# Optimization experiments

Measured on AMD Instinct MI355X. Metric: run time of the kernel, lower is better.

## Reference

```python
import jax, jax.numpy as jnp
import numpy as np

B, NPG, H, TD, NF, NL, A = 64, 20, 512, 256, 128, 6, 100
N = B * NPG
E = B * NPG * (NPG - 1)
ANG_LO, ANG_HI = 59.9, 120.1
LOG_MEANS = jnp.array([1.575442910194397, 1.7017393112182617, 1.9781638383865356], jnp.float32)
LOG_STDS = jnp.array([0.24437622725963593, 0.26526379585266113, 0.3535512685775757], jnp.float32)
TWO_PI = 2.0 * np.pi


def _logmap(x, y):
    z = TWO_PI * (y - x)
    return jnp.arctan2(jnp.sin(z), jnp.cos(z)) / TWO_PI


def _lattice_matrix(lengths, angles_deg):
    a = jnp.deg2rad(angles_deg)
    c, s = jnp.cos(a), jnp.sin(a)
    val = jnp.clip((c[:, 0] * c[:, 1] - c[:, 2]) / (s[:, 0] * s[:, 1]), -1.0, 1.0)
    gs = jnp.arccos(val)
    zero = jnp.zeros_like(lengths[:, 0])
    va = jnp.stack([lengths[:, 0] * s[:, 1], zero, lengths[:, 0] * c[:, 1]], 1)
    vb = jnp.stack([-lengths[:, 1] * s[:, 0] * jnp.cos(gs), lengths[:, 1] * s[:, 0] * jnp.sin(gs), lengths[:, 1] * c[:, 0]], 1)
    vc = jnp.stack([zero, zero, lengths[:, 2]], 1)
    return jnp.stack([va, vb, vc], 1)


def _ln(x, g, b, eps=1e-5):
    mu = jnp.mean(x, -1, keepdims=True)
    var = jnp.var(x, -1, keepdims=True)
    return (x - mu) * jax.lax.rsqrt(var + eps) * g + b


def setup_inputs() -> dict:
    key = jax.random.key(0)
    ks = jax.random.split(key, 24)
    # forward data
    t = jax.random.uniform(ks[0], (B, 1), jnp.float32)
    atom_types = jax.random.randint(ks[1], (N,), 1, A + 1, jnp.int32)
    frac_coords = jax.random.uniform(ks[2], (N, 3), jnp.float32)
    lattice_params = 0.5 * jax.random.normal(ks[3], (B, 6), jnp.float32)
    num_atoms = jnp.full((B,), NPG, jnp.int32)
    node2graph = jnp.repeat(jnp.arange(B, dtype=jnp.int32), NPG)
    # fully-connected edges per graph, no self edges (static structure)
    loc = np.arange(NPG)
    src_l, dst_l = np.meshgrid(loc, loc, indexing='ij')
    mask = src_l != dst_l
    src_l, dst_l = src_l[mask], dst_l[mask]  # (NPG*(NPG-1),)
    offs = (np.arange(B)[:, None] * NPG)
    src = (offs + src_l[None, :]).reshape(-1)
    dst = (offs + dst_l[None, :]).reshape(-1)
    edge_index = jnp.asarray(np.stack([src, dst]), jnp.int32)  # (2, E)
    edge2graph = node2graph[edge_index[0]]
    # parameters
    def w(k, shape, fan_in):
        return (jax.random.normal(k, shape, jnp.float32) / np.sqrt(fan_in)).astype(jnp.float32)
    EIN = 3 + 3 * H + 6 + NF * 2 * 3  # 2313
    p = {
        'W_node': w(ks[4], (A, H), A),
        'W_time': w(ks[5], (1, TD), 1),
        'W_latent': w(ks[6], (H + TD, H), H + TD),
        'ln_gamma': jnp.ones((NL, H), jnp.float32),
        'ln_beta': jnp.zeros((NL, H), jnp.float32),
        'We1': w(ks[7], (NL, EIN, H), EIN),
        'be1': jnp.zeros((NL, H), jnp.float32),
        'We2': w(ks[8], (NL, H, H), H),
        'be2': jnp.zeros((NL, H), jnp.float32),
        'Wn1': w(ks[9], (NL, 2 * H, H), 2 * H),
        'bn1': jnp.zeros((NL, H), jnp.float32),
        'Wn2': w(ks[10], (NL, H, H), H),
        'bn2': jnp.zeros((NL, H), jnp.float32),
        'W_numatom': w(ks[11], (NL, A, H), A),
        'fln_gamma': jnp.ones((H,), jnp.float32),
        'fln_beta': jnp.zeros((H,), jnp.float32),
        'W_coord': w(ks[12], (H, 3), H),
        'W_latout': w(ks[13], (2 * H, 6), 2 * H),
        'b_latout': jnp.zeros((6,), jnp.float32),
    }
    return dict(t=t, frac_coords=frac_coords, lattice_params=lattice_params,
                atom_types=atom_types, num_atoms=num_atoms, node2graph=node2graph,
                edge_index=edge_index, edge2graph=edge2graph, **p)


def reference(t, frac_coords, lattice_params, W_node, W_time, W_latent, ln_gamma, ln_beta,
              We1, be1, We2, be2, Wn1, bn1, Wn2, bn2, W_numatom, fln_gamma, fln_beta,
              W_coord, W_latout, b_latout, atom_types, num_atoms, node2graph, edge_index, edge2graph):
    n_nodes = frac_coords.shape[0]
    n_graphs = t.shape[0]
    src, dst = edge_index[0], edge_index[1]
    frac_diff = _logmap(frac_coords[src], frac_coords[dst])  # (E,3)

    atom_oh = jax.nn.one_hot(jnp.clip(atom_types - 1, 0), A, dtype=jnp.float32)
    h = atom_oh @ W_node
    temb = t @ W_time  # (B,TD)
    h = jnp.concatenate([h, temb[node2graph]], -1) @ W_latent

    lattice_flat = lattice_params  # 6-D in directly
    lengths = jnp.exp(lattice_params[:, :3] * LOG_STDS + LOG_MEANS)
    angles_deg = ANG_LO + (ANG_HI - ANG_LO) * jax.nn.sigmoid(lattice_params[:, 3:])
    Lmat = _lattice_matrix(lengths, angles_deg)  # (B,3,3)
    ltl = jnp.einsum('bij,bkj->bik', Lmat, Lmat)  # L @ L^T

    dots = jnp.einsum('eij,ej->ei', ltl[edge2graph], frac_diff)
    unit_dots = dots / (jnp.linalg.norm(dots, axis=-1, keepdims=True) + 1e-12)

    freqs = TWO_PI * jnp.arange(NF, dtype=jnp.float32)
    emb = (frac_diff[..., None] * freqs).reshape(-1, 3 * NF)
    femb = jnp.concatenate([jnp.sin(emb), jnp.cos(emb)], -1)  # (E, 768)

    na_oh = jax.nn.one_hot(num_atoms - 1, A, dtype=jnp.float32)  # (B,100)
    lat_e = lattice_flat[edge2graph]
    counts = jnp.maximum(jax.ops.segment_sum(jnp.ones_like(src, dtype=jnp.float32), src, num_segments=n_nodes), 1.0)[:, None]

    for l in range(NL):
        h_in = h
        hn = _ln(h_in, ln_gamma[l], ln_beta[l])
        na_emb = (na_oh @ W_numatom[l])[edge2graph]
        ef = jnp.concatenate([unit_dots, hn[src], hn[dst], lat_e, femb, na_emb], -1)
        e = jax.nn.silu(jax.nn.silu(ef @ We1[l] + be1[l]) @ We2[l] + be2[l])
        agg = jax.ops.segment_sum(e, src, num_segments=n_nodes) / counts
        out = jax.nn.silu(jax.nn.silu(jnp.concatenate([hn, agg], -1) @ Wn1[l] + bn1[l]) @ Wn2[l] + bn2[l])
        h = h_in + out

    h = _ln(h, fln_gamma, fln_beta)
    pos_v = h @ W_coord  # (N,3)
    sum_pool = jax.ops.segment_sum(h, node2graph, num_segments=n_graphs)
    mean_pool = sum_pool / num_atoms.astype(jnp.float32)[:, None]
    cell_v = jnp.concatenate([mean_pool, sum_pool], -1) @ W_latout + b_latout  # (B,6)
    return pos_v, cell_v
```

## Files before the change

### kernel.cpp

```cpp
#include <hip/hip_runtime.h>
#include <hip/hip_bf16.h>

typedef __hip_bfloat16 bf16;
typedef __attribute__((ext_vector_type(8))) __bf16 bf16x8;
typedef __attribute__((ext_vector_type(4))) float f32x4;

#define B_   64
#define NPG_ 20
#define H_   512
#define TD_  256
#define NF_  128
#define NL_  6
#define A_   100
#define N_   (B_ * NPG_)
#define E_   (B_ * NPG_ * (NPG_-1))
#define EIN_ 2313

__device__ __forceinline__ float bf2f(bf16 x) { return __bfloat162float(x); }
__device__ __forceinline__ bf16  f2bf(float x) { return __float2bfloat16(x); }
__device__ __forceinline__ float siluf(float x) { return x / (1.0f + expf(-x)); }
__device__ __forceinline__ float ldf(const void* p, size_t i, int isb) {
    return isb ? bf2f(((const bf16*)p)[i]) : ((const float*)p)[i];
}
__device__ __forceinline__ void async_cp16(const bf16* src, bf16* dst) {
    __builtin_amdgcn_global_load_lds(
        (const __attribute__((address_space(1))) unsigned int*)src,
        (__attribute__((address_space(3))) unsigned int*)dst,
        16, 0, 0);
}

__global__ void detect_dtype(const unsigned int* __restrict__ tw, int* __restrict__ flag) {
    if (threadIdx.x != 0) return;
    int cnt = 0;
    for (int i = 0; i < 32; i++) {
        unsigned b1 = (tw[i] >> 8) & 0xFF;
        if (b1 >= 0x20 && b1 < 0x40) cnt++;
    }
    *flag = (cnt >= 16) ? 1 : 0;
}

__global__ void ws_sentinel(bf16* out) { if (threadIdx.x == 0) out[0] = f2bf(1000.0f); }

__global__ void prep_graph(const void* __restrict__ latp, float* __restrict__ ltl,
                           const int* __restrict__ flag) {
    int b = threadIdx.x;
    if (b >= B_) return;
    int isb = *flag;
    const float LM[3] = {1.575442910194397f, 1.7017393112182617f, 1.9781638383865356f};
    const float LS[3] = {0.24437622725963593f, 0.26526379585266113f, 0.3535512685775757f};
    float lp[6];
    for (int i = 0; i < 6; i++) lp[i] = ldf(latp, b*6 + i, isb);
    float len[3], c[3], s[3];
    for (int i = 0; i < 3; i++) len[i] = expf(lp[i] * LS[i] + LM[i]);
    for (int i = 0; i < 3; i++) {
        float sig = 1.0f / (1.0f + expf(-lp[3+i]));
        float deg = 59.9f + 60.2f * sig;
        float a = deg * 0.017453292519943295f;
        c[i] = cosf(a); s[i] = sinf(a);
    }
    float val = (c[0]*c[1] - c[2]) / (s[0]*s[1]);
    val = fminf(1.0f, fmaxf(-1.0f, val));
    float gs = acosf(val);
    float L[3][3];
    L[0][0] = len[0]*s[1]; L[0][1] = 0.0f;               L[0][2] = len[0]*c[1];
    L[1][0] = -len[1]*s[0]*cosf(gs); L[1][1] = len[1]*s[0]*sinf(gs); L[1][2] = len[1]*c[0];
    L[2][0] = 0.0f; L[2][1] = 0.0f; L[2][2] = len[2];
    for (int i = 0; i < 3; i++)
        for (int k = 0; k < 3; k++)
            ltl[b*9 + i*3 + k] = L[i][0]*L[k][0] + L[i][1]*L[k][1] + L[i][2]*L[k][2];
}

__global__ __launch_bounds__(512) void prep_q(const void* __restrict__ W_time,
                                              const void* __restrict__ W_latent,
                                              float* __restrict__ q,
                                              const int* __restrict__ flag) {
    int j = threadIdx.x;
    int isb = *flag;
    float s0 = 0.0f, s1 = 0.0f, s2 = 0.0f, s3 = 0.0f;
    for (int d = 0; d < TD_; d += 4) {
        s0 += ldf(W_time, d+0, isb) * ldf(W_latent, (size_t)(H_ + d+0)*H_ + j, isb);
        s1 += ldf(W_time, d+1, isb) * ldf(W_latent, (size_t)(H_ + d+1)*H_ + j, isb);
        s2 += ldf(W_time, d+2, isb) * ldf(W_latent, (size_t)(H_ + d+2)*H_ + j, isb);
        s3 += ldf(W_time, d+3, isb) * ldf(W_latent, (size_t)(H_ + d+3)*H_ + j, isb);
    }
    q[j] = (s0 + s1) + (s2 + s3);
}

__global__ __launch_bounds__(256) void pq_gather(const void* __restrict__ W_node,
                                                 const void* __restrict__ W_numatom,
                                                 bf16* __restrict__ PQa,
                                                 const int* __restrict__ flag) {
    int z = blockIdx.x, ch = blockIdx.y;
    int isb = *flag;
    int base = ch * 4096;
    for (int idx = base + threadIdx.x; idx < base + 4096; idx += 256) {
        int r = idx >> 9, c = idx & 511;
        float v = 0.0f;
        if (r < A_) {
            if (z == 0) v = ldf(W_node, (size_t)r*512 + c, isb);
            else        v = ldf(W_numatom, ((size_t)(z-1)*A_ + r)*512 + c, isb);
        }
        PQa[(size_t)z*65536 + idx] = f2bf(v);
    }
}

__global__ __launch_bounds__(256) void transpose_pq(const void* __restrict__ W_latent,
                                                    const void* __restrict__ We1,
                                                    bf16* __restrict__ PQbt,
                                                    const int* __restrict__ flag) {
    __shared__ bf16 tile[32][33];
    int z = blockIdx.z;
    int isb = *flag;
    const void* src = (z == 0) ? W_latent : We1;
    size_t off = (z == 0) ? 0 : ((size_t)(z-1)*EIN_ + 1801)*512;
    bf16* dst = PQbt + (size_t)z*512*512;
    int r0 = blockIdx.y * 32, c0 = blockIdx.x * 32;
    #pragma unroll
    for (int i = 0; i < 32; i += 8)
        tile[threadIdx.y + i][threadIdx.x] =
            f2bf(ldf(src, off + (size_t)(r0 + threadIdx.y + i)*512 + c0 + threadIdx.x, isb));
    __syncthreads();
    #pragma unroll
    for (int i = 0; i < 32; i += 8)
        dst[(size_t)(c0 + threadIdx.y + i)*512 + r0 + threadIdx.x] = tile[threadIdx.x][threadIdx.y + i];
}

__global__ __launch_bounds__(256) void transpose_layer(
    const void* __restrict__ We1p, const void* __restrict__ We2p,
    const void* __restrict__ Wn1p, const void* __restrict__ Wn2p, size_t l,
    bf16* __restrict__ WtAB, bf16* __restrict__ Wtf, bf16* __restrict__ Wte2,
    bf16* __restrict__ Wtn1, bf16* __restrict__ Wtn2,
    const int* __restrict__ flag) {
    __shared__ bf16 tile[32][33];
    int which = blockIdx.z;
    int isb = *flag;
    const void* src; size_t off; bf16* dst; int R;
    switch (which) {
        case 0:  src = We1p; off = (l*EIN_ + 3)*512;    dst = WtAB;            R = 512;  break;
        case 1:  src = We1p; off = (l*EIN_ + 515)*512;  dst = WtAB + 512*512;  R = 512;  break;
        case 2:  src = We1p; off = (l*EIN_ + 1033)*512; dst = Wtf;             R = 768;  break;
        case 3:  src = We2p; off = l*512*512;           dst = Wte2;            R = 512;  break;
        case 4:  src = Wn1p; off = l*1024*512;          dst = Wtn1;            R = 1024; break;
        default: src = Wn2p; off = l*512*512;           dst = Wtn2;            R = 512;  break;
    }
    int r0 = blockIdx.y * 32, c0 = blockIdx.x * 32;
    if (r0 >= R) return;
    #pragma unroll
    for (int i = 0; i < 32; i += 8)
        tile[threadIdx.y + i][threadIdx.x] =
            f2bf(ldf(src, off + (size_t)(r0 + threadIdx.y + i)*512 + c0 + threadIdx.x, isb));
    __syncthreads();
    #pragma unroll
    for (int i = 0; i < 32; i += 8)
        dst[(size_t)(c0 + threadIdx.y + i)*R + r0 + threadIdx.x] = tile[threadIdx.x][threadIdx.y + i];
}

__global__ __launch_bounds__(512) void node_embed_fast(const bf16* __restrict__ P,
                                                       const float* __restrict__ q,
                                                       const void* __restrict__ t,
                                                       const int* __restrict__ atom_types,
                                                       const int* __restrict__ node2graph,
                                                       float* __restrict__ h,
                                                       const int* __restrict__ flag) {
    int i = blockIdx.x, j = threadIdx.x;
    int isb = *flag;
    int at = atom_types[i] - 1; if (at < 0) at = 0;
    float pv = (at < A_) ? bf2f(P[(size_t)at*512 + j]) : 0.0f;
    float tv = ldf(t, node2graph[i], isb);
    h[(size_t)i*H_ + j] = pv + tv * q[j];
}

__global__ __launch_bounds__(384) void edge_prep(const void* __restrict__ frac,
                                                 const int* __restrict__ edge_index,
                                                 const int* __restrict__ e2g,
                                                 const void* __restrict__ latp,
                                                 const int* __restrict__ num_atoms,
                                                 const float* __restrict__ ltl,
                                                 float* __restrict__ edat,
                                                 bf16* __restrict__ femb,
                                                 const int* __restrict__ flag) {
    const float TWO_PI_F = 6.283185307179586f;
    int e = blockIdx.x;
    int isb = *flag;
    int src = edge_index[e], dst = edge_index[E_ + e];
    int tid = threadIdx.x;
    int d = tid >> 7, k = tid & 127;
    float x = ldf(frac, src*3 + d, isb), y = ldf(frac, dst*3 + d, isb);
    float diff = y - x;
    float fd = diff - rintf(diff);
    float sv, cv;
    sincosf(fd * (TWO_PI_F * (float)k), &sv, &cv);
    femb[(size_t)e*768 + d*NF_ + k]       = f2bf(sv);
    femb[(size_t)e*768 + 384 + d*NF_ + k] = f2bf(cv);
    if (tid < 3) {
        int g = e2g[e];
        float f3[3];
        for (int dd = 0; dd < 3; dd++) {
            float df = ldf(frac, dst*3 + dd, isb) - ldf(frac, src*3 + dd, isb);
            f3[dd] = df - rintf(df);
        }
        float dots[3];
        for (int i = 0; i < 3; i++)
            dots[i] = ltl[g*9 + i*3 + 0]*f3[0] + ltl[g*9 + i*3 + 1]*f3[1] + ltl[g*9 + i*3 + 2]*f3[2];
        float nrm = sqrtf(dots[0]*dots[0] + dots[1]*dots[1] + dots[2]*dots[2]);
        edat[(size_t)e*16 + tid] = dots[tid] / (nrm + 1e-12f);
        if (tid == 0) {
            for (int i = 0; i < 6; i++) edat[(size_t)e*16 + 3 + i] = ldf(latp, g*6 + i, isb);
            int na = num_atoms[g] - 1;
            if (na < 0 || na >= A_) na = -1;
            edat[(size_t)e*16 + 9]  = __int_as_float(src);
            edat[(size_t)e*16 + 10] = __int_as_float(dst);
            edat[(size_t)e*16 + 11] = __int_as_float(na);
        }
    }
}

__device__ __forceinline__ float block_sum_256(float v, float* red) {
    for (int o = 32; o; o >>= 1) v += __shfl_down(v, o);
    int w = threadIdx.x >> 6, lane = threadIdx.x & 63;
    if (lane == 0) red[w] = v;
    __syncthreads();
    float s = red[0] + red[1] + red[2] + red[3];
    __syncthreads();
    return s;
}

__global__ __launch_bounds__(256) void ln_kernel(const float* __restrict__ x,
                                                 const void* __restrict__ gamma,
                                                 const void* __restrict__ beta, size_t goff,
                                                 bf16* __restrict__ cat,
                                                 const int* __restrict__ flag) {
    __shared__ float red[4];
    size_t n = blockIdx.x;
    int tid = threadIdx.x;
    int isb = *flag;
    const float* xr = x + n*H_;
    float v0 = xr[tid], v1 = xr[tid + 256];
    float mu = block_sum_256(v0 + v1, red) * (1.0f/512.0f);
    float d0 = v0 - mu, d1 = v1 - mu;
    float var = block_sum_256(d0*d0 + d1*d1, red) * (1.0f/512.0f);
    float rs = 1.0f / sqrtf(var + 1e-5f);
    cat[n*1024 + tid]       = f2bf(d0*rs*ldf(gamma, goff + tid, isb)       + ldf(beta, goff + tid, isb));
    cat[n*1024 + 256 + tid] = f2bf(d1*rs*ldf(gamma, goff + tid + 256, isb) + ldf(beta, goff + tid + 256, isb));
}

template<int EPI, int TM>
__global__ __launch_bounds__(256) void gemm_bt(
        const bf16* __restrict__ A, int lda,
        const bf16* __restrict__ Bt,
        const void* __restrict__ bias, size_t boff,
        bf16* __restrict__ Cb, float* __restrict__ Cf,
        int K, int N,
        size_t zsA, size_t zsB, size_t zsC,
        const int* __restrict__ flag,
        const bf16* __restrict__ hnAB, const bf16* __restrict__ Qc,
        const float* __restrict__ edat,
        const void* __restrict__ We1, size_t lidx) {
    constexpr int MT = TM / 32;
    __shared__ __align__(16) bf16 As[TM*64];
    __shared__ __align__(16) bf16 Bs[128*64];
    const int z = blockIdx.z;
    A  += (size_t)z * zsA;
    Bt += (size_t)z * zsB;
    const size_t coff = (size_t)z * zsC;
    const int tid = threadIdx.x;
    const int wave = tid >> 6, lane = tid & 63;
    const int lrow = lane & 15, lq = lane >> 4;
    const size_t m0 = (size_t)blockIdx.y * TM;
    const int n0 = blockIdx.x * 128;
    const int wm = (wave >> 1) * (TM/2), wn = (wave & 1) * 64;
    const int ar = lane >> 3;
    const int gk = (lane & 7) ^ ar;
    f32x4 acc[MT][4] = {};

    for (int k0 = 0; k0 < K; k0 += 64) {
        if (k0) __syncthreads();
        #pragma unroll
        for (int i = 0; i < TM/32; i++) {
            int R = wave*(TM/4) + i*8;
            async_cp16(A + (m0 + R + ar)*lda + k0 + gk*8, As + R*64);
        }
        #pragma unroll
        for (int i = 0; i < 4; i++) {
            int R = wave*32 + i*8;
            async_cp16(Bt + (size_t)(n0 + R + ar)*K + k0 + gk*8, Bs + R*64);
        }
        __syncthreads();
        #pragma unroll
        for (int kk = 0; kk < 2; kk++) {
            bf16x8 af[MT], bfr[4];
            #pragma unroll
            for (int mt = 0; mt < MT; mt++) {
                int r = wm + mt*16 + lrow;
                int p = (kk*4 + lq) ^ (r & 7);
                af[mt] = *(const bf16x8*)(As + r*64 + p*8);
            }
            #pragma unroll
            for (int nt = 0; nt < 4; nt++) {
                int r = wn + nt*16 + lrow;
                int p = (kk*4 + lq) ^ (r & 7);
                bfr[nt] = *(const bf16x8*)(Bs + r*64 + p*8);
            }
            #pragma unroll
            for (int mt = 0; mt < MT; mt++)
                #pragma unroll
                for (int nt = 0; nt < 4; nt++)
                    acc[mt][nt] = __builtin_amdgcn_mfma_f32_16x16x32_bf16(af[mt], bfr[nt], acc[mt][nt], 0, 0, 0);
        }
    }

    if constexpr (EPI == 3) {
        const int isb = *flag;
        float w9[4][9], b1v[4];
        #pragma unroll
        for (int nt = 0; nt < 4; nt++) {
            int col = n0 + wn + nt*16 + lrow;
            size_t wb = lidx*EIN_*512 + col;
            w9[nt][0] = ldf(We1, wb + 0*512, isb);
            w9[nt][1] = ldf(We1, wb + 1*512, isb);
            w9[nt][2] = ldf(We1, wb + 2*512, isb);
            #pragma unroll
            for (int i = 0; i < 6; i++) w9[nt][3+i] = ldf(We1, wb + (size_t)(1027+i)*512, isb);
            b1v[nt] = ldf(bias, boff + col, isb);
        }
        #pragma unroll
        for (int mt = 0; mt < MT; mt++) {
            #pragma unroll
            for (int r = 0; r < 4; r++) {
                size_t e = m0 + wm + mt*16 + lq*4 + r;
                const float4* ed = (const float4*)(edat + e*16);
                float4 q0 = ed[0], q1 = ed[1], q2 = ed[2];
                int se = __float_as_int(q2.y), de = __float_as_int(q2.z), na = __float_as_int(q2.w);
                #pragma unroll
                for (int nt = 0; nt < 4; nt++) {
                    int col = n0 + wn + nt*16 + lrow;
                    float x = acc[mt][nt][r] + b1v[nt]
                            + bf2f(hnAB[(size_t)se*1024 + col])
                            + bf2f(hnAB[(size_t)de*1024 + 512 + col])
                            + (na >= 0 ? bf2f(Qc[(size_t)(1+lidx)*65536 + (size_t)na*512 + col]) : 0.0f)
                            + q0.x*w9[nt][0] + q0.y*w9[nt][1] + q0.z*w9[nt][2]
                            + q0.w*w9[nt][3] + q1.x*w9[nt][4] + q1.y*w9[nt][5]
                            + q1.z*w9[nt][6] + q1.w*w9[nt][7] + q2.x*w9[nt][8];
                    Cb[e*512 + col] = f2bf(siluf(x));
                }
            }
        }
    } else {
        const int isb = bias ? *flag : 0;
        #pragma unroll
        for (int mt = 0; mt < MT; mt++)
            #pragma unroll
            for (int nt = 0; nt < 4; nt++) {
                int col = n0 + wn + nt*16 + lrow;
                float bv = bias ? ldf(bias, boff + col, isb) : 0.0f;
                #pragma unroll
                for (int r = 0; r < 4; r++) {
                    size_t row = m0 + wm + mt*16 + lq*4 + r;
                    float x = acc[mt][nt][r] + bv;
                    if (EPI == 0)      Cb[coff + row*N + col] = f2bf(x);
                    else if (EPI == 1) Cb[coff + row*N + col] = f2bf(siluf(x));
                    else               Cf[coff + row*N + col] += siluf(x);
                }
            }
    }
}

__global__ __launch_bounds__(256) void seg_mean(const bf16* __restrict__ e2,
                                                bf16* __restrict__ cat) {
    int n = blockIdx.x;
    #pragma unroll
    for (int jj = 0; jj < 2; jj++) {
        int j = threadIdx.x + jj*256;
        const bf16* base = e2 + (size_t)n*19*H_ + j;
        float s = 0.0f;
        #pragma unroll
        for (int i = 0; i < 19; i++) s += bf2f(base[(size_t)i*H_]);
        cat[(size_t)n*1024 + 512 + j] = f2bf(s / 19.0f);
    }
}

__global__ __launch_bounds__(256) void pos_out(const bf16* __restrict__ hln,
                                               const void* __restrict__ W_coord,
                                               void* __restrict__ out,
                                               const int* __restrict__ flag) {
    int wave = threadIdx.x >> 6, lane = threadIdx.x & 63;
    int n = blockIdx.x*4 + wave;
    int isb = *flag;
    float s0 = 0, s1 = 0, s2 = 0;
    for (int k = lane; k < H_; k += 64) {
        float hv = bf2f(hln[(size_t)n*1024 + k]);
        s0 += hv * ldf(W_coord, k*3 + 0, isb);
        s1 += hv * ldf(W_coord, k*3 + 1, isb);
        s2 += hv * ldf(W_coord, k*3 + 2, isb);
    }
    for (int o = 32; o; o >>= 1) {
        s0 += __shfl_down(s0, o); s1 += __shfl_down(s1, o); s2 += __shfl_down(s2, o);
    }
    if (lane == 0) {
        if (isb) { bf16* o = (bf16*)out;  o[n*3] = f2bf(s0); o[n*3+1] = f2bf(s1); o[n*3+2] = f2bf(s2); }
        else     { float* o = (float*)out; o[n*3] = s0; o[n*3+1] = s1; o[n*3+2] = s2; }
    }
}

__global__ __launch_bounds__(512) void cell_out(const bf16* __restrict__ hln,
                                                const void* __restrict__ W_latout,
                                                const void* __restrict__ b_latout,
                                                const int* __restrict__ num_atoms,
                                                void* __restrict__ out,
                                                const int* __restrict__ flag) {
    __shared__ float red[8*6];
    int b = blockIdx.x, j = threadIdx.x;
    int isb = *flag;
    float s = 0.0f;
    for (int i = 0; i < NPG_; i++) s += bf2f(hln[(size_t)(b*NPG_ + i)*1024 + j]);
    float m = s / (float)num_atoms[b];
    float p[6];
    #pragma unroll
    for (int c = 0; c < 6; c++)
        p[c] = m * ldf(W_latout, j*6 + c, isb) + s * ldf(W_latout, (512 + j)*6 + c, isb);
    int w = j >> 6, lane = j & 63;
    #pragma unroll
    for (int c = 0; c < 6; c++) {
        float v = p[c];
        for (int o = 32; o; o >>= 1) v += __shfl_down(v, o);
        if (lane == 0) red[w*6 + c] = v;
    }
    __syncthreads();
    if (j < 6) {
        float v = 0.0f;
        for (int w2 = 0; w2 < 8; w2++) v += red[w2*6 + j];
        float r = v + ldf(b_latout, j, isb);
        if (isb) ((bf16*)out)[N_*3 + b*6 + j] = f2bf(r);
        else     ((float*)out)[N_*3 + b*6 + j] = r;
    }
}

extern "C" void kernel_launch(void* const* d_in, const int* in_sizes, int n_in,
                              void* d_out, int out_size, void* d_ws, size_t ws_size,
                              hipStream_t stream) {
    const void* t          = d_in[0];
    const void* frac       = d_in[1];
    const void* latp       = d_in[2];
    const int*  atom_types = (const int*)d_in[3];
    const int*  num_atoms  = (const int*)d_in[4];
    const int*  node2graph = (const int*)d_in[5];
    const int*  edge_index = (const int*)d_in[6];
    const int*  e2g        = (const int*)d_in[7];
    const void* W_node     = d_in[8];
    const void* W_time     = d_in[9];
    const void* W_latent   = d_in[10];
    const void* ln_gamma   = d_in[11];
    const void* ln_beta    = d_in[12];
    const void* We1        = d_in[13];
    const void* be1        = d_in[14];
    const void* We2        = d_in[15];
    const void* be2        = d_in[16];
    const void* Wn1        = d_in[17];
    const void* bn1        = d_in[18];
    const void* Wn2        = d_in[19];
    const void* bn2        = d_in[20];
    const void* W_numatom  = d_in[21];
    const void* fln_gamma  = d_in[22];
    const void* fln_beta   = d_in[23];
    const void* W_coord    = d_in[24];
    const void* W_latout   = d_in[25];
    const void* b_latout   = d_in[26];

    char* p = (char*)d_ws;
    auto alloc = [&](size_t bytes) { char* r = p; p += (bytes + 255) & ~(size_t)255; return r; };
    int*   flag  = (int*)alloc(4);
    float* ltl   = (float*)alloc((size_t)B_*9*4);
    float* q     = (float*)alloc((size_t)H_*4);
    float* h     = (float*)alloc((size_t)N_*H_*4);
    float* edat  = (float*)alloc((size_t)E_*16*4);
    bf16* hnAB  = (bf16*)alloc((size_t)N_*1024*2);
    bf16* femb  = (bf16*)alloc((size_t)E_*768*2);
    bf16* e1    = (bf16*)alloc((size_t)E_*H_*2);
    bf16* e2    = (bf16*)alloc((size_t)E_*H_*2);
    bf16* cat   = (bf16*)alloc((size_t)N_*1024*2);
    bf16* n1s   = (bf16*)alloc((size_t)N_*H_*2);
    bf16* PQc   = (bf16*)alloc((size_t)7*128*512*2);
    bf16* WtAB  = (bf16*)alloc((size_t)1024*512*2);
    bf16* Wtf   = (bf16*)alloc((size_t)512*768*2);
    bf16* Wte2  = (bf16*)alloc((size_t)512*512*2);
    bf16* Wtn1  = (bf16*)alloc((size_t)512*1024*2);
    bf16* Wtn2  = (bf16*)alloc((size_t)512*512*2);
    bf16* PQa   = e1;
    bf16* PQbt  = e2;

    if ((size_t)(p - (char*)d_ws) > ws_size) {
        ws_sentinel<<<1, 64, 0, stream>>>((bf16*)d_out);
        return;
    }

    detect_dtype<<<1, 64, 0, stream>>>((const unsigned int*)t, flag);
    prep_graph<<<1, 64, 0, stream>>>(latp, ltl, flag);
    prep_q<<<1, 512, 0, stream>>>(W_time, W_latent, q, flag);
    pq_gather<<<dim3(7, 16), 256, 0, stream>>>(W_node, W_numatom, PQa, flag);
    transpose_pq<<<dim3(16, 16, 7), dim3(32, 8), 0, stream>>>(W_latent, We1, PQbt, flag);
    gemm_bt<0,128><<<dim3(4, 1, 7), 256, 0, stream>>>(
        PQa, 512, PQbt, nullptr, 0, PQc, nullptr, 512, 512,
        (size_t)128*512, (size_t)512*512, (size_t)128*512,
        flag, nullptr, nullptr, nullptr, nullptr, 0);
    node_embed_fast<<<N_, 512, 0, stream>>>(PQc, q, t, atom_types, node2graph, h, flag);
    edge_prep<<<E_, 384, 0, stream>>>(frac, edge_index, e2g, latp, num_atoms, ltl, edat, femb, flag);

    for (size_t l = 0; l < NL_; l++) {
        transpose_layer<<<dim3(16, 32, 6), dim3(32, 8), 0, stream>>>(
            We1, We2, Wn1, Wn2, l, WtAB, Wtf, Wte2, Wtn1, Wtn2, flag);
        ln_kernel<<<N_, 256, 0, stream>>>(h, ln_gamma, ln_beta, l*H_, cat, flag);
        gemm_bt<0,64><<<dim3(8, N_/64), 256, 0, stream>>>(
            cat, 1024, WtAB, nullptr, 0, hnAB, nullptr, 512, 1024, 0, 0, 0,
            flag, nullptr, nullptr, nullptr, nullptr, 0);
        gemm_bt<3,128><<<dim3(4, E_/128), 256, 0, stream>>>(
            femb, 768, Wtf, be1, l*H_, e1, nullptr, 768, 512, 0, 0, 0,
            flag, hnAB, PQc, edat, We1, l);
        gemm_bt<1,128><<<dim3(4, E_/128), 256, 0, stream>>>(
            e1, 512, Wte2, be2, l*H_, e2, nullptr, 512, 512, 0, 0, 0,
            flag, nullptr, nullptr, nullptr, nullptr, 0);
        seg_mean<<<N_, 256, 0, stream>>>(e2, cat);
        gemm_bt<1,64><<<dim3(4, N_/64), 256, 0, stream>>>(
            cat, 1024, Wtn1, bn1, l*H_, n1s, nullptr, 1024, 512, 0, 0, 0,
            flag, nullptr, nullptr, nullptr, nullptr, 0);
        gemm_bt<2,64><<<dim3(4, N_/64), 256, 0, stream>>>(
            n1s, 512, Wtn2, bn2, l*H_, nullptr, h, 512, 512, 0, 0, 0,
            flag, nullptr, nullptr, nullptr, nullptr, 0);
    }

    ln_kernel<<<N_, 256, 0, stream>>>(h, fln_gamma, fln_beta, 0, cat, flag);
    pos_out<<<N_/4, 256, 0, stream>>>(cat, W_coord, d_out, flag);
    cell_out<<<B_, 512, 0, stream>>>(cat, W_latout, b_latout, num_atoms, d_out, flag);
}
```

Measured before the change: 1.223 ms.

## Fold small edge features into femb GEMM K dimension and shrink edge tiles

```diff
diff --git a/kernel.cpp b/kernel.cpp
--- a/kernel.cpp
+++ b/kernel.cpp
@@ -15,6 +15,7 @@
 #define N_   (B_ * NPG_)
 #define E_   (B_ * NPG_ * (NPG_-1))
 #define EIN_ 2313
+#define KF_  832
 
 __device__ __forceinline__ float bf2f(bf16 x) { return __bfloat162float(x); }
 __device__ __forceinline__ bf16  f2bf(float x) { return __float2bfloat16(x); }
@@ -134,14 +135,14 @@
     __shared__ bf16 tile[32][33];
     int which = blockIdx.z;
     int isb = *flag;
-    const void* src; size_t off; bf16* dst; int R;
+    const void* src; size_t off; bf16* dst; int R; int ldd;
     switch (which) {
-        case 0:  src = We1p; off = (l*EIN_ + 3)*512;    dst = WtAB;            R = 512;  break;
-        case 1:  src = We1p; off = (l*EIN_ + 515)*512;  dst = WtAB + 512*512;  R = 512;  break;
-        case 2:  src = We1p; off = (l*EIN_ + 1033)*512; dst = Wtf;             R = 768;  break;
-        case 3:  src = We2p; off = l*512*512;           dst = Wte2;            R = 512;  break;
-        case 4:  src = Wn1p; off = l*1024*512;          dst = Wtn1;            R = 1024; break;
-        default: src = Wn2p; off = l*512*512;           dst = Wtn2;            R = 512;  break;
+        case 0:  src = We1p; off = (l*EIN_ + 3)*512;    dst = WtAB;            R = 512;  ldd = 512;  break;
+        case 1:  src = We1p; off = (l*EIN_ + 515)*512;  dst = WtAB + 512*512;  R = 512;  ldd = 512;  break;
+        case 2:  src = We1p; off = (l*EIN_ + 1033)*512; dst = Wtf;             R = 768;  ldd = KF_;  break;
+        case 3:  src = We2p; off = l*512*512;           dst = Wte2;            R = 512;  ldd = 512;  break;
+        case 4:  src = Wn1p; off = l*1024*512;          dst = Wtn1;            R = 1024; ldd = 1024; break;
+        default: src = Wn2p; off = l*512*512;           dst = Wtn2;            R = 512;  ldd = 512;  break;
     }
     int r0 = blockIdx.y * 32, c0 = blockIdx.x * 32;
     if (r0 >= R) return;
@@ -152,7 +153,20 @@
     __syncthreads();
     #pragma unroll
     for (int i = 0; i < 32; i += 8)
-        dst[(size_t)(c0 + threadIdx.y + i)*R + r0 + threadIdx.x] = tile[threadIdx.x][threadIdx.y + i];
+        dst[(size_t)(c0 + threadIdx.y + i)*ldd + r0 + threadIdx.x] = tile[threadIdx.x][threadIdx.y + i];
+}
+
+__global__ __launch_bounds__(512) void wtf_tail(const void* __restrict__ We1, size_t l,
+                                                bf16* __restrict__ Wtf,
+                                                const int* __restrict__ flag) {
+    int n = threadIdx.x;
+    int isb = *flag;
+    const int rows[9] = {0, 1, 2, 1027, 1028, 1029, 1030, 1031, 1032};
+    #pragma unroll
+    for (int j = 0; j < 64; j++) {
+        float v = (j < 9) ? ldf(We1, (l*EIN_ + rows[j])*512 + n, isb) : 0.0f;
+        Wtf[(size_t)n*KF_ + 768 + j] = f2bf(v);
+    }
 }
 
 __global__ __launch_bounds__(512) void node_embed_fast(const bf16* __restrict__ P,
@@ -176,7 +190,7 @@
                                                  const void* __restrict__ latp,
                                                  const int* __restrict__ num_atoms,
                                                  const float* __restrict__ ltl,
-                                                 float* __restrict__ edat,
+                                                 int* __restrict__ edat,
                                                  bf16* __restrict__ femb,
                                                  const int* __restrict__ flag) {
     const float TWO_PI_F = 6.283185307179586f;
@@ -190,27 +204,33 @@
     float fd = diff - rintf(diff);
     float sv, cv;
     sincosf(fd * (TWO_PI_F * (float)k), &sv, &cv);
-    femb[(size_t)e*768 + d*NF_ + k]       = f2bf(sv);
-    femb[(size_t)e*768 + 384 + d*NF_ + k] = f2bf(cv);
-    if (tid < 3) {
+    femb[(size_t)e*KF_ + d*NF_ + k]       = f2bf(sv);
+    femb[(size_t)e*KF_ + 384 + d*NF_ + k] = f2bf(cv);
+    if (tid < 64) {
         int g = e2g[e];
-        float f3[3];
-        for (int dd = 0; dd < 3; dd++) {
-            float df = ldf(frac, dst*3 + dd, isb) - ldf(frac, src*3 + dd, isb);
-            f3[dd] = df - rintf(df);
-        }
-        float dots[3];
-        for (int i = 0; i < 3; i++)
-            dots[i] = ltl[g*9 + i*3 + 0]*f3[0] + ltl[g*9 + i*3 + 1]*f3[1] + ltl[g*9 + i*3 + 2]*f3[2];
-        float nrm = sqrtf(dots[0]*dots[0] + dots[1]*dots[1] + dots[2]*dots[2]);
-        edat[(size_t)e*16 + tid] = dots[tid] / (nrm + 1e-12f);
+        float v = 0.0f;
+        if (tid < 3) {
+            float f3[3];
+            for (int dd = 0; dd < 3; dd++) {
+                float df = ldf(frac, dst*3 + dd, isb) - ldf(frac, src*3 + dd, isb);
+                f3[dd] = df - rintf(df);
+            }
+            float dots[3];
+            for (int i = 0; i < 3; i++)
+                dots[i] = ltl[g*9 + i*3 + 0]*f3[0] + ltl[g*9 + i*3 + 1]*f3[1] + ltl[g*9 + i*3 + 2]*f3[2];
+            float nrm = sqrtf(dots[0]*dots[0] + dots[1]*dots[1] + dots[2]*dots[2]);
+            v = dots[tid] / (nrm + 1e-12f);
+        } else if (tid < 9) {
+            v = ldf(latp, g*6 + tid - 3, isb);
+        }
+        femb[(size_t)e*KF_ + 768 + tid] = f2bf(v);
         if (tid == 0) {
-            for (int i = 0; i < 6; i++) edat[(size_t)e*16 + 3 + i] = ldf(latp, g*6 + i, isb);
             int na = num_atoms[g] - 1;
             if (na < 0 || na >= A_) na = -1;
-            edat[(size_t)e*16 + 9]  = __int_as_float(src);
-            edat[(size_t)e*16 + 10] = __int_as_float(dst);
-            edat[(size_t)e*16 + 11] = __int_as_float(na);
+            edat[e*4 + 0] = src;
+            edat[e*4 + 1] = dst;
+            edat[e*4 + 2] = na;
+            edat[e*4 + 3] = 0;
         }
     }
 }
@@ -254,8 +274,7 @@
         size_t zsA, size_t zsB, size_t zsC,
         const int* __restrict__ flag,
         const bf16* __restrict__ hnAB, const bf16* __restrict__ Qc,
-        const float* __restrict__ edat,
-        const void* __restrict__ We1, size_t lidx) {
+        const int* __restrict__ edat, size_t lidx) {
     constexpr int MT = TM / 32;
     __shared__ __align__(16) bf16 As[TM*64];
     __shared__ __align__(16) bf16 Bs[128*64];
@@ -311,36 +330,24 @@
 
     if constexpr (EPI == 3) {
         const int isb = *flag;
-        float w9[4][9], b1v[4];
-        #pragma unroll
-        for (int nt = 0; nt < 4; nt++) {
-            int col = n0 + wn + nt*16 + lrow;
-            size_t wb = lidx*EIN_*512 + col;
-            w9[nt][0] = ldf(We1, wb + 0*512, isb);
-            w9[nt][1] = ldf(We1, wb + 1*512, isb);
-            w9[nt][2] = ldf(We1, wb + 2*512, isb);
-            #pragma unroll
-            for (int i = 0; i < 6; i++) w9[nt][3+i] = ldf(We1, wb + (size_t)(1027+i)*512, isb);
-            b1v[nt] = ldf(bias, boff + col, isb);
-        }
+        float b1v[4];
+        #pragma unroll
+        for (int nt = 0; nt < 4; nt++)
+            b1v[nt] = ldf(bias, boff + n0 + wn + nt*16 + lrow, isb);
         #pragma unroll
         for (int mt = 0; mt < MT; mt++) {
             #pragma unroll
             for (int r = 0; r < 4; r++) {
                 size_t e = m0 + wm + mt*16 + lq*4 + r;
-                const float4* ed = (const float4*)(edat + e*16);
-                float4 q0 = ed[0], q1 = ed[1], q2 = ed[2];
-                int se = __float_as_int(q2.y), de = __float_as_int(q2.z), na = __float_as_int(q2.w);
+                const int4 q = *(const int4*)(edat + e*4);
+                int se = q.x, de = q.y, na = q.z;
                 #pragma unroll
                 for (int nt = 0; nt < 4; nt++) {
                     int col = n0 + wn + nt*16 + lrow;
                     float x = acc[mt][nt][r] + b1v[nt]
                             + bf2f(hnAB[(size_t)se*1024 + col])
                             + bf2f(hnAB[(size_t)de*1024 + 512 + col])
-                            + (na >= 0 ? bf2f(Qc[(size_t)(1+lidx)*65536 + (size_t)na*512 + col]) : 0.0f)
-                            + q0.x*w9[nt][0] + q0.y*w9[nt][1] + q0.z*w9[nt][2]
-                            + q0.w*w9[nt][3] + q1.x*w9[nt][4] + q1.y*w9[nt][5]
-                            + q1.z*w9[nt][6] + q1.w*w9[nt][7] + q2.x*w9[nt][8];
+                            + (na >= 0 ? bf2f(Qc[(size_t)(1+lidx)*65536 + (size_t)na*512 + col]) : 0.0f);
                     Cb[e*512 + col] = f2bf(siluf(x));
                 }
             }
@@ -472,16 +479,16 @@
     float* ltl   = (float*)alloc((size_t)B_*9*4);
     float* q     = (float*)alloc((size_t)H_*4);
     float* h     = (float*)alloc((size_t)N_*H_*4);
-    float* edat  = (float*)alloc((size_t)E_*16*4);
+    int*   edat  = (int*)alloc((size_t)E_*4*4);
     bf16* hnAB  = (bf16*)alloc((size_t)N_*1024*2);
-    bf16* femb  = (bf16*)alloc((size_t)E_*768*2);
+    bf16* femb  = (bf16*)alloc((size_t)E_*KF_*2);
     bf16* e1    = (bf16*)alloc((size_t)E_*H_*2);
     bf16* e2    = (bf16*)alloc((size_t)E_*H_*2);
     bf16* cat   = (bf16*)alloc((size_t)N_*1024*2);
     bf16* n1s   = (bf16*)alloc((size_t)N_*H_*2);
     bf16* PQc   = (bf16*)alloc((size_t)7*128*512*2);
     bf16* WtAB  = (bf16*)alloc((size_t)1024*512*2);
-    bf16* Wtf   = (bf16*)alloc((size_t)512*768*2);
+    bf16* Wtf   = (bf16*)alloc((size_t)512*KF_*2);
     bf16* Wte2  = (bf16*)alloc((size_t)512*512*2);
     bf16* Wtn1  = (bf16*)alloc((size_t)512*1024*2);
     bf16* Wtn2  = (bf16*)alloc((size_t)512*512*2);
@@ -501,30 +508,31 @@
     gemm_bt<0,128><<<dim3(4, 1, 7), 256, 0, stream>>>(
         PQa, 512, PQbt, nullptr, 0, PQc, nullptr, 512, 512,
         (size_t)128*512, (size_t)512*512, (size_t)128*512,
-        flag, nullptr, nullptr, nullptr, nullptr, 0);
+        flag, nullptr, nullptr, nullptr, 0);
     node_embed_fast<<<N_, 512, 0, stream>>>(PQc, q, t, atom_types, node2graph, h, flag);
     edge_prep<<<E_, 384, 0, stream>>>(frac, edge_index, e2g, latp, num_atoms, ltl, edat, femb, flag);
 
     for (size_t l = 0; l < NL_; l++) {
         transpose_layer<<<dim3(16, 32, 6), dim3(32, 8), 0, stream>>>(
             We1, We2, Wn1, Wn2, l, WtAB, Wtf, Wte2, Wtn1, Wtn2, flag);
+        wtf_tail<<<1, 512, 0, stream>>>(We1, l, Wtf, flag);
         ln_kernel<<<N_, 256, 0, stream>>>(h, ln_gamma, ln_beta, l*H_, cat, flag);
         gemm_bt<0,64><<<dim3(8, N_/64), 256, 0, stream>>>(
             cat, 1024, WtAB, nullptr, 0, hnAB, nullptr, 512, 1024, 0, 0, 0,
-            flag, nullptr, nullptr, nullptr, nullptr, 0);
-        gemm_bt<3,128><<<dim3(4, E_/128), 256, 0, stream>>>(
-            femb, 768, Wtf, be1, l*H_, e1, nullptr, 768, 512, 0, 0, 0,
-            flag, hnAB, PQc, edat, We1, l);
-        gemm_bt<1,128><<<dim3(4, E_/128), 256, 0, stream>>>(
+            flag, nullptr, nullptr, nullptr, 0);
+        gemm_bt<3,64><<<dim3(4, E_/64), 256, 0, stream>>>(
+            femb, KF_, Wtf, be1, l*H_, e1, nullptr, KF_, 512, 0, 0, 0,
+            flag, hnAB, PQc, edat, l);
+        gemm_bt<1,64><<<dim3(4, E_/64), 256, 0, stream>>>(
             e1, 512, Wte2, be2, l*H_, e2, nullptr, 512, 512, 0, 0, 0,
-            flag, nullptr, nullptr, nullptr, nullptr, 0);
+            flag, nullptr, nullptr, nullptr, 0);
         seg_mean<<<N_, 256, 0, stream>>>(e2, cat);
         gemm_bt<1,64><<<dim3(4, N_/64), 256, 0, stream>>>(
             cat, 1024, Wtn1, bn1, l*H_, n1s, nullptr, 1024, 512, 0, 0, 0,
-            flag, nullptr, nullptr, nullptr, nullptr, 0);
+            flag, nullptr, nullptr, nullptr, 0);
         gemm_bt<2,64><<<dim3(4, N_/64), 256, 0, stream>>>(
             n1s, 512, Wtn2, bn2, l*H_, nullptr, h, 512, 512, 0, 0, 0,
-            flag, nullptr, nullptr, nullptr, nullptr, 0);
+            flag, nullptr, nullptr, nullptr, 0);
     }
 
     ln_kernel<<<N_, 256, 0, stream>>>(h, fln_gamma, fln_beta, 0, cat, flag);
```

New measurement: 1.189 ms. 1.03x faster.
